# Optimization experiments

Hardware: AMD Instinct MI355X
Metric: run time of the kernel (lower is better)

Reference implementation:

```python
import jax, jax.numpy as jnp
import numpy as np
from jax import lax

N_TRACES = 128
TRACE_LEN = 32          # uniform trace length -> seq_len
INPUT_DIM = 64
HIDDEN_DIM = 128
BATCH = N_TRACES * TRACE_LEN  # 4096 events = batch_size


def setup_inputs() -> dict:
    key = jax.random.key(0)
    ks = jax.random.split(key, 12)
    s = 1.0 / np.sqrt(HIDDEN_DIM)
    u = lambda k, shape: jax.random.uniform(k, shape, jnp.float32, -s, s)
    return {
        "input": jax.random.normal(ks[0], (BATCH, INPUT_DIM), jnp.float32),
        # layer 0 LSTM params (gate order i,f,g,o as in torch)
        "W_ih0": u(ks[1], (4 * HIDDEN_DIM, INPUT_DIM)),
        "W_hh0": u(ks[2], (4 * HIDDEN_DIM, HIDDEN_DIM)),
        "b_ih0": u(ks[3], (4 * HIDDEN_DIM,)),
        "b_hh0": u(ks[4], (4 * HIDDEN_DIM,)),
        # layer 1 LSTM params
        "W_ih1": u(ks[5], (4 * HIDDEN_DIM, HIDDEN_DIM)),
        "W_hh1": u(ks[6], (4 * HIDDEN_DIM, HIDDEN_DIM)),
        "b_ih1": u(ks[7], (4 * HIDDEN_DIM,)),
        "b_hh1": u(ks[8], (4 * HIDDEN_DIM,)),
        # final linear: hidden -> 1
        "W_lin": u(ks[9], (1, HIDDEN_DIM)),
        "b_lin": u(ks[10], (1,)),
    }


def _lstm_layer(xs, W_ih, W_hh, b_ih, b_hh):
    # xs: [T, B, D_in] time-major. Returns hidden stream [T, B, H].
    H = W_hh.shape[1]
    B = xs.shape[1]
    # precompute input projection for all timesteps
    x_proj = jnp.einsum('tbd,gd->tbg', xs, W_ih) + b_ih + b_hh  # [T,B,4H]

    def step(carry, xp):
        h, c = carry
        gates = xp + h @ W_hh.T                # [B,4H]
        i, f, g, o = jnp.split(gates, 4, axis=-1)
        i = jax.nn.sigmoid(i)
        f = jax.nn.sigmoid(f)
        g = jnp.tanh(g)
        o = jax.nn.sigmoid(o)
        c = f * c + i * g
        h = o * jnp.tanh(c)
        return (h, c), h

    h0 = jnp.zeros((B, H), xs.dtype)
    _, hs = lax.scan(step, (h0, h0), x_proj)
    return hs


def _forward(input, W_ih0, W_hh0, b_ih0, b_hh0, W_ih1, W_hh1, b_ih1, b_hh1, W_lin, b_lin):
    L, D = TRACE_LEN, INPUT_DIM
    # Prefix scatter: event k of a trace gets the padded prefix events[0..k].
    x_tr = input.reshape(N_TRACES, L, D)                       # [Ntr, L, D]
    causal = (jnp.arange(L)[None, :] <= jnp.arange(L)[:, None])  # [k, j] mask j<=k
    padded = x_tr[:, None, :, :] * causal[None, :, :, None].astype(input.dtype)  # [Ntr,L(k),L(j),D]
    padded = padded.reshape(BATCH, L, D)                       # batch-first padded sequences

    xs = jnp.transpose(padded, (1, 0, 2))                      # [L, B, D] time-major
    h1 = _lstm_layer(xs, W_ih0, W_hh0, b_ih0, b_hh0)           # [L, B, H]
    h2 = _lstm_layer(h1, W_ih1, W_hh1, b_ih1, b_hh1)           # [L, B, H]

    out = jnp.einsum('tbh,oh->tbo', h2, W_lin) + b_lin         # [L, B, 1]
    # last valid timestep gather: lengths[i]-1 = (i mod L)
    lens_m1 = jnp.tile(jnp.arange(L), N_TRACES)                # [B]
    y_pred = out[lens_m1, jnp.arange(BATCH), 0]                # [B]
    return y_pred


def reference(input, W_ih0, W_hh0, b_ih0, b_hh0, W_ih1, W_hh1, b_ih1, b_hh1, W_lin, b_lin):
    return _forward(input, W_ih0, W_hh0, b_ih0, b_hh0, W_ih1, W_hh1, b_ih1, b_hh1, W_lin, b_lin)
```

## Files before the change

kernel.cpp:

```cpp
#include <hip/hip_runtime.h>

#define N_TRACES 128
#define TLEN 32
#define IN_DIM 64
#define HID 128
#define G4 (4 * HID)
#define BATCH (N_TRACES * TLEN)


__device__ __forceinline__ float fast_sigmoid(float x) {
    return 1.0f / (1.0f + __expf(-x));
}
__device__ __forceinline__ float fast_tanh(float x) {
    return 1.0f - 2.0f / (__expf(2.0f * x) + 1.0f);
}
__device__ __forceinline__ float quad_reduce(float x) {
    x += __int_as_float(__builtin_amdgcn_update_dpp(
        0, __float_as_int(x), 0xB1 , 0xF, 0xF, true));
    x += __int_as_float(__builtin_amdgcn_update_dpp(
        0, __float_as_int(x), 0x4E , 0xF, 0xF, true));
    return x;
}


template <int K>
__global__ __launch_bounds__(256) void gemm_bt(
    const float* __restrict__ A,
    const float* __restrict__ W,
    const float* __restrict__ b1,
    const float* __restrict__ b2,
    float* __restrict__ out,
    int Nld)
{
    constexpr int LD = 68;
    __shared__ float At[K][LD];
    __shared__ float Wt[K][LD];

    const int tid = threadIdx.x;
    const int m0 = blockIdx.x * 64;
    const int n0 = blockIdx.y * 64;

    #pragma unroll
    for (int j = 0; j < K / 16; ++j) {
        const int e = 4 * (tid + 256 * j);
        const int row = e / K;
        const int k = e % K;
        float4 va = *(const float4*)(A + (size_t)(m0 + row) * K + k);
        At[k + 0][row] = va.x; At[k + 1][row] = va.y;
        At[k + 2][row] = va.z; At[k + 3][row] = va.w;
        float4 vw = *(const float4*)(W + (size_t)(n0 + row) * K + k);
        Wt[k + 0][row] = vw.x; Wt[k + 1][row] = vw.y;
        Wt[k + 2][row] = vw.z; Wt[k + 3][row] = vw.w;
    }
    __syncthreads();

    const int tx = tid & 15;
    const int ty = tid >> 4;
    float acc[4][4] = {};

    #pragma unroll 4
    for (int k = 0; k < K; ++k) {
        float4 a = *(const float4*)&At[k][ty * 4];
        float4 w = *(const float4*)&Wt[k][tx * 4];
        acc[0][0] = fmaf(a.x, w.x, acc[0][0]); acc[0][1] = fmaf(a.x, w.y, acc[0][1]);
        acc[0][2] = fmaf(a.x, w.z, acc[0][2]); acc[0][3] = fmaf(a.x, w.w, acc[0][3]);
        acc[1][0] = fmaf(a.y, w.x, acc[1][0]); acc[1][1] = fmaf(a.y, w.y, acc[1][1]);
        acc[1][2] = fmaf(a.y, w.z, acc[1][2]); acc[1][3] = fmaf(a.y, w.w, acc[1][3]);
        acc[2][0] = fmaf(a.z, w.x, acc[2][0]); acc[2][1] = fmaf(a.z, w.y, acc[2][1]);
        acc[2][2] = fmaf(a.z, w.z, acc[2][2]); acc[2][3] = fmaf(a.z, w.w, acc[2][3]);
        acc[3][0] = fmaf(a.w, w.x, acc[3][0]); acc[3][1] = fmaf(a.w, w.y, acc[3][1]);
        acc[3][2] = fmaf(a.w, w.z, acc[3][2]); acc[3][3] = fmaf(a.w, w.w, acc[3][3]);
    }

    float bb[4];
    #pragma unroll
    for (int j = 0; j < 4; ++j) {
        const int n = n0 + tx * 4 + j;
        bb[j] = b1[n] + b2[n];
    }
    #pragma unroll
    for (int i = 0; i < 4; ++i) {
        const int m = m0 + ty * 4 + i;
        float4 v;
        v.x = acc[i][0] + bb[0]; v.y = acc[i][1] + bb[1];
        v.z = acc[i][2] + bb[2]; v.w = acc[i][3] + bb[3];
        *(float4*)(out + (size_t)m * Nld + n0 + tx * 4) = v;
    }
}


__global__ __launch_bounds__(512) void lstm_rec(
    const float* __restrict__ xproj,
    const float* __restrict__ Whh,
    float* __restrict__ hout)
{
    const int trace = blockIdx.x;
    const int tid = threadIdx.x;
    const int u = tid >> 2;
    const int s = tid & 3;

    float w[4][32];
    #pragma unroll
    for (int i = 0; i < 4; ++i) {
        const float* wr = Whh + (size_t)(u + 128 * i) * HID + 32 * s;
        #pragma unroll
        for (int j = 0; j < 8; ++j) {
            float4 v = *(const float4*)(wr + 4 * j);
            w[i][4 * j + 0] = v.x; w[i][4 * j + 1] = v.y;
            w[i][4 * j + 2] = v.z; w[i][4 * j + 3] = v.w;
        }
    }

    __shared__ float hbuf[2][144];
    if (tid < 144) { hbuf[0][tid] = 0.0f; hbuf[1][tid] = 0.0f; }

    const float* xpb = xproj + (size_t)trace * TLEN * G4;
    float* hob = hout + (size_t)trace * TLEN * HID;

    float xp[4] = {0.f, 0.f, 0.f, 0.f};
    if (s == 0) {
        #pragma unroll
        for (int i = 0; i < 4; ++i) xp[i] = xpb[u + 128 * i];
    }
    float c = 0.0f;
    __syncthreads();

    #pragma unroll 1
    for (int t = 0; t < TLEN; ++t) {
        const float* hb = &hbuf[t & 1][36 * s];
        float hv[32];
        #pragma unroll
        for (int j = 0; j < 8; ++j) {
            float4 v = *(const float4*)(hb + 4 * j);
            hv[4 * j + 0] = v.x; hv[4 * j + 1] = v.y;
            hv[4 * j + 2] = v.z; hv[4 * j + 3] = v.w;
        }

        float xn[4] = {0.f, 0.f, 0.f, 0.f};
        if (s == 0 && t + 1 < TLEN) {
            #pragma unroll
            for (int i = 0; i < 4; ++i) xn[i] = xpb[(t + 1) * G4 + u + 128 * i];
        }

        float acc0 = 0.f, acc1 = 0.f, acc2 = 0.f, acc3 = 0.f;
        #pragma unroll
        for (int j = 0; j < 32; ++j) {
            acc0 = fmaf(w[0][j], hv[j], acc0);
            acc1 = fmaf(w[1][j], hv[j], acc1);
            acc2 = fmaf(w[2][j], hv[j], acc2);
            acc3 = fmaf(w[3][j], hv[j], acc3);
        }
        acc0 = quad_reduce(acc0);
        acc1 = quad_reduce(acc1);
        acc2 = quad_reduce(acc2);
        acc3 = quad_reduce(acc3);

        if (s == 0) {
            const float iv = fast_sigmoid(acc0 + xp[0]);
            const float fv = fast_sigmoid(acc1 + xp[1]);
            const float gv = fast_tanh(acc2 + xp[2]);
            const float ov = fast_sigmoid(acc3 + xp[3]);
            c = fv * c + iv * gv;
            const float h = ov * fast_tanh(c);
            hbuf[(t + 1) & 1][u + 4 * (u >> 5)] = h;
            hob[t * HID + u] = h;
            xp[0] = xn[0]; xp[1] = xn[1]; xp[2] = xn[2]; xp[3] = xn[3];
        }
        __syncthreads();
    }
}


__global__ __launch_bounds__(256) void rowdot(
    const float* __restrict__ A,
    const float* __restrict__ wl,
    const float* __restrict__ bl,
    float* __restrict__ y)
{
    const int r = blockIdx.x * 256 + threadIdx.x;
    const float4* a4 = (const float4*)(A + (size_t)r * HID);
    const float4* w4 = (const float4*)wl;
    float sacc = 0.f;
    #pragma unroll
    for (int j = 0; j < HID / 4; ++j) {
        float4 a = a4[j], w = w4[j];
        sacc = fmaf(a.x, w.x, sacc);
        sacc = fmaf(a.y, w.y, sacc);
        sacc = fmaf(a.z, w.z, sacc);
        sacc = fmaf(a.w, w.w, sacc);
    }
    y[r] = sacc + bl[0];
}


extern "C" void kernel_launch(void* const* d_in, const int* in_sizes, int n_in,
                              void* d_out, int out_size, void* d_ws, size_t ws_size,
                              hipStream_t stream) {
    const float* input = (const float*)d_in[0];
    const float* W_ih0 = (const float*)d_in[1];
    const float* W_hh0 = (const float*)d_in[2];
    const float* b_ih0 = (const float*)d_in[3];
    const float* b_hh0 = (const float*)d_in[4];
    const float* W_ih1 = (const float*)d_in[5];
    const float* W_hh1 = (const float*)d_in[6];
    const float* b_ih1 = (const float*)d_in[7];
    const float* b_hh1 = (const float*)d_in[8];
    const float* W_lin = (const float*)d_in[9];
    const float* b_lin = (const float*)d_in[10];
    float* out = (float*)d_out;

    float* xproj = (float*)d_ws;
    float* h1 = xproj + (size_t)BATCH * G4;
    float* h2 = h1 + (size_t)BATCH * HID;

    dim3 ggrid(BATCH / 64, G4 / 64);

    gemm_bt<IN_DIM><<<ggrid, 256, 0, stream>>>(input, W_ih0, b_ih0, b_hh0, xproj, G4);
    lstm_rec<<<N_TRACES, 512, 0, stream>>>(xproj, W_hh0, h1);
    gemm_bt<HID><<<ggrid, 256, 0, stream>>>(h1, W_ih1, b_ih1, b_hh1, xproj, G4);
    lstm_rec<<<N_TRACES, 512, 0, stream>>>(xproj, W_hh1, h2);
    rowdot<<<BATCH / 256, 256, 0, stream>>>(h2, W_lin, b_lin, out);
}
```

Measured before the change: 180.2 us.

## Fuse both LSTM layers, layer-1 input projection and final linear into one per-trace kernel

Replaces the layer-0 recurrence, the layer-1 GEMM, the layer-1 recurrence and the rowdot with a single per-trace kernel. Hidden states and the layer-1 input projection stay in shared memory instead of going through global memory, and the separate launches go away. The GEMM's LDS transpose stores are also rotated per thread to reduce bank conflicts. The trade-off is that the layer-1 projection now runs as a matvec over only 128 blocks rather than a wide GEMM, and the kernel uses about 82KB of shared memory per block, which lowers occupancy.

Result: faster. 170.9 us (-5.1%).

```diff
diff --git a/kernel.cpp b/kernel.cpp
--- a/kernel.cpp
+++ b/kernel.cpp
@@ -20,6 +20,35 @@
     x += __int_as_float(__builtin_amdgcn_update_dpp(
         0, __float_as_int(x), 0x4E , 0xF, 0xF, true));
     return x;
+}
+
+__device__ __forceinline__ void load_w(const float* __restrict__ W, int u, int s,
+                                       float (&w)[4][32]) {
+    #pragma unroll
+    for (int i = 0; i < 4; ++i) {
+        const float* wr = W + (size_t)(u + 128 * i) * HID + 32 * s;
+        #pragma unroll
+        for (int j = 0; j < 8; ++j) {
+            float4 v = *(const float4*)(wr + 4 * j);
+            w[i][4 * j + 0] = v.x; w[i][4 * j + 1] = v.y;
+            w[i][4 * j + 2] = v.z; w[i][4 * j + 3] = v.w;
+        }
+    }
+}
+
+__device__ __forceinline__ void matvec_acc(const float (&w)[4][32],
+                                           const float* hb, float (&acc)[4]) {
+    #pragma unroll
+    for (int j = 0; j < 8; ++j) {
+        float4 v = *(const float4*)(hb + 4 * j);
+        float hx[4] = {v.x, v.y, v.z, v.w};
+        #pragma unroll
+        for (int e = 0; e < 4; ++e) {
+            #pragma unroll
+            for (int i = 0; i < 4; ++i)
+                acc[i] = fmaf(w[i][4 * j + e], hx[e], acc[i]);
+        }
+    }
 }
 
 
@@ -40,17 +69,22 @@
     const int m0 = blockIdx.x * 64;
     const int n0 = blockIdx.y * 64;
 
+    const int rot = tid & 3;
     #pragma unroll
     for (int j = 0; j < K / 16; ++j) {
         const int e = 4 * (tid + 256 * j);
         const int row = e / K;
         const int k = e % K;
         float4 va = *(const float4*)(A + (size_t)(m0 + row) * K + k);
-        At[k + 0][row] = va.x; At[k + 1][row] = va.y;
-        At[k + 2][row] = va.z; At[k + 3][row] = va.w;
         float4 vw = *(const float4*)(W + (size_t)(n0 + row) * K + k);
-        Wt[k + 0][row] = vw.x; Wt[k + 1][row] = vw.y;
-        Wt[k + 2][row] = vw.z; Wt[k + 3][row] = vw.w;
+        float fa[4] = {va.x, va.y, va.z, va.w};
+        float fw[4] = {vw.x, vw.y, vw.z, vw.w};
+        #pragma unroll
+        for (int ii = 0; ii < 4; ++ii) {
+            const int i = (ii + rot) & 3;
+            At[k + i][row] = fa[i];
+            Wt[k + i][row] = fw[i];
+        }
     }
     __syncthreads();
 
@@ -89,107 +123,123 @@
 }
 
 
-__global__ __launch_bounds__(512) void lstm_rec(
-    const float* __restrict__ xproj,
-    const float* __restrict__ Whh,
-    float* __restrict__ hout)
+__global__ __launch_bounds__(512, 2) void fused_trace(
+    const float* __restrict__ xproj0,
+    const float* __restrict__ Whh0,
+    const float* __restrict__ Wih1,
+    const float* __restrict__ bih1,
+    const float* __restrict__ bhh1,
+    const float* __restrict__ Whh1,
+    const float* __restrict__ Wlin,
+    const float* __restrict__ blin,
+    float* __restrict__ y)
 {
     const int trace = blockIdx.x;
     const int tid = threadIdx.x;
     const int u = tid >> 2;
     const int s = tid & 3;
+    const int pu = u + 4 * (u >> 5);
+
+    __shared__ float hs[TLEN][140];
+    __shared__ float xp1[TLEN][G4];
 
     float w[4][32];
-    #pragma unroll
-    for (int i = 0; i < 4; ++i) {
-        const float* wr = Whh + (size_t)(u + 128 * i) * HID + 32 * s;
-        #pragma unroll
-        for (int j = 0; j < 8; ++j) {
-            float4 v = *(const float4*)(wr + 4 * j);
-            w[i][4 * j + 0] = v.x; w[i][4 * j + 1] = v.y;
-            w[i][4 * j + 2] = v.z; w[i][4 * j + 3] = v.w;
-        }
-    }
-
-    __shared__ float hbuf[2][144];
-    if (tid < 144) { hbuf[0][tid] = 0.0f; hbuf[1][tid] = 0.0f; }
-
-    const float* xpb = xproj + (size_t)trace * TLEN * G4;
-    float* hob = hout + (size_t)trace * TLEN * HID;
-
+
+    load_w(Whh0, u, s, w);
+    const float* xpb = xproj0 + (size_t)trace * TLEN * G4;
     float xp[4] = {0.f, 0.f, 0.f, 0.f};
     if (s == 0) {
         #pragma unroll
         for (int i = 0; i < 4; ++i) xp[i] = xpb[u + 128 * i];
     }
     float c = 0.0f;
-    __syncthreads();
-
     #pragma unroll 1
     for (int t = 0; t < TLEN; ++t) {
-        const float* hb = &hbuf[t & 1][36 * s];
-        float hv[32];
-        #pragma unroll
-        for (int j = 0; j < 8; ++j) {
-            float4 v = *(const float4*)(hb + 4 * j);
-            hv[4 * j + 0] = v.x; hv[4 * j + 1] = v.y;
-            hv[4 * j + 2] = v.z; hv[4 * j + 3] = v.w;
-        }
+        float acc[4] = {0.f, 0.f, 0.f, 0.f};
+        if (t > 0) matvec_acc(w, &hs[t - 1][36 * s], acc);
 
         float xn[4] = {0.f, 0.f, 0.f, 0.f};
         if (s == 0 && t + 1 < TLEN) {
             #pragma unroll
             for (int i = 0; i < 4; ++i) xn[i] = xpb[(t + 1) * G4 + u + 128 * i];
         }
-
-        float acc0 = 0.f, acc1 = 0.f, acc2 = 0.f, acc3 = 0.f;
-        #pragma unroll
-        for (int j = 0; j < 32; ++j) {
-            acc0 = fmaf(w[0][j], hv[j], acc0);
-            acc1 = fmaf(w[1][j], hv[j], acc1);
-            acc2 = fmaf(w[2][j], hv[j], acc2);
-            acc3 = fmaf(w[3][j], hv[j], acc3);
-        }
-        acc0 = quad_reduce(acc0);
-        acc1 = quad_reduce(acc1);
-        acc2 = quad_reduce(acc2);
-        acc3 = quad_reduce(acc3);
+        #pragma unroll
+        for (int i = 0; i < 4; ++i) acc[i] = quad_reduce(acc[i]);
 
         if (s == 0) {
-            const float iv = fast_sigmoid(acc0 + xp[0]);
-            const float fv = fast_sigmoid(acc1 + xp[1]);
-            const float gv = fast_tanh(acc2 + xp[2]);
-            const float ov = fast_sigmoid(acc3 + xp[3]);
+            const float iv = fast_sigmoid(acc[0] + xp[0]);
+            const float fv = fast_sigmoid(acc[1] + xp[1]);
+            const float gv = fast_tanh(acc[2] + xp[2]);
+            const float ov = fast_sigmoid(acc[3] + xp[3]);
             c = fv * c + iv * gv;
-            const float h = ov * fast_tanh(c);
-            hbuf[(t + 1) & 1][u + 4 * (u >> 5)] = h;
-            hob[t * HID + u] = h;
+            hs[t][pu] = ov * fast_tanh(c);
             xp[0] = xn[0]; xp[1] = xn[1]; xp[2] = xn[2]; xp[3] = xn[3];
         }
         __syncthreads();
     }
-}
-
-
-__global__ __launch_bounds__(256) void rowdot(
-    const float* __restrict__ A,
-    const float* __restrict__ wl,
-    const float* __restrict__ bl,
-    float* __restrict__ y)
-{
-    const int r = blockIdx.x * 256 + threadIdx.x;
-    const float4* a4 = (const float4*)(A + (size_t)r * HID);
-    const float4* w4 = (const float4*)wl;
-    float sacc = 0.f;
-    #pragma unroll
-    for (int j = 0; j < HID / 4; ++j) {
-        float4 a = a4[j], w = w4[j];
-        sacc = fmaf(a.x, w.x, sacc);
-        sacc = fmaf(a.y, w.y, sacc);
-        sacc = fmaf(a.z, w.z, sacc);
-        sacc = fmaf(a.w, w.w, sacc);
-    }
-    y[r] = sacc + bl[0];
+
+    load_w(Wih1, u, s, w);
+    float bi[4] = {0.f, 0.f, 0.f, 0.f};
+    if (s == 0) {
+        #pragma unroll
+        for (int i = 0; i < 4; ++i) bi[i] = bih1[u + 128 * i] + bhh1[u + 128 * i];
+    }
+    #pragma unroll 1
+    for (int t = 0; t < TLEN; ++t) {
+        float acc[4] = {0.f, 0.f, 0.f, 0.f};
+        matvec_acc(w, &hs[t][36 * s], acc);
+        #pragma unroll
+        for (int i = 0; i < 4; ++i) acc[i] = quad_reduce(acc[i]);
+        if (s == 0) {
+            #pragma unroll
+            for (int i = 0; i < 4; ++i) xp1[t][u + 128 * i] = acc[i] + bi[i];
+        }
+    }
+    __syncthreads();
+
+    load_w(Whh1, u, s, w);
+    c = 0.0f;
+    #pragma unroll 1
+    for (int t = 0; t < TLEN; ++t) {
+        float acc[4] = {0.f, 0.f, 0.f, 0.f};
+        if (t > 0) matvec_acc(w, &hs[t - 1][36 * s], acc);
+        #pragma unroll
+        for (int i = 0; i < 4; ++i) acc[i] = quad_reduce(acc[i]);
+
+        if (s == 0) {
+            const float iv = fast_sigmoid(acc[0] + xp1[t][u]);
+            const float fv = fast_sigmoid(acc[1] + xp1[t][u + 128]);
+            const float gv = fast_tanh(acc[2] + xp1[t][u + 256]);
+            const float ov = fast_sigmoid(acc[3] + xp1[t][u + 384]);
+            c = fv * c + iv * gv;
+            hs[t][pu] = ov * fast_tanh(c);
+        }
+        __syncthreads();
+    }
+
+    if (tid < 128) {
+        const int tq = tid >> 2;
+        const int sq = tid & 3;
+        float wl[32];
+        #pragma unroll
+        for (int j = 0; j < 8; ++j) {
+            float4 v = *(const float4*)(Wlin + 32 * sq + 4 * j);
+            wl[4 * j + 0] = v.x; wl[4 * j + 1] = v.y;
+            wl[4 * j + 2] = v.z; wl[4 * j + 3] = v.w;
+        }
+        const float* hb = &hs[tq][36 * sq];
+        float a = 0.f;
+        #pragma unroll
+        for (int j = 0; j < 8; ++j) {
+            float4 v = *(const float4*)(hb + 4 * j);
+            a = fmaf(v.x, wl[4 * j + 0], a);
+            a = fmaf(v.y, wl[4 * j + 1], a);
+            a = fmaf(v.z, wl[4 * j + 2], a);
+            a = fmaf(v.w, wl[4 * j + 3], a);
+        }
+        a = quad_reduce(a);
+        if (sq == 0) y[trace * TLEN + tq] = a + blin[0];
+    }
 }
 
 
@@ -209,15 +259,11 @@
     const float* b_lin = (const float*)d_in[10];
     float* out = (float*)d_out;
 
-    float* xproj = (float*)d_ws;
-    float* h1 = xproj + (size_t)BATCH * G4;
-    float* h2 = h1 + (size_t)BATCH * HID;
+    float* xproj0 = (float*)d_ws;
 
     dim3 ggrid(BATCH / 64, G4 / 64);
 
-    gemm_bt<IN_DIM><<<ggrid, 256, 0, stream>>>(input, W_ih0, b_ih0, b_hh0, xproj, G4);
-    lstm_rec<<<N_TRACES, 512, 0, stream>>>(xproj, W_hh0, h1);
-    gemm_bt<HID><<<ggrid, 256, 0, stream>>>(h1, W_ih1, b_ih1, b_hh1, xproj, G4);
-    lstm_rec<<<N_TRACES, 512, 0, stream>>>(xproj, W_hh1, h2);
-    rowdot<<<BATCH / 256, 256, 0, stream>>>(h2, W_lin, b_lin, out);
-}
+    gemm_bt<IN_DIM><<<ggrid, 256, 0, stream>>>(input, W_ih0, b_ih0, b_hh0, xproj0, G4);
+    fused_trace<<<N_TRACES, 512, 0, stream>>>(xproj0, W_hh0, W_ih1, b_ih1, b_hh1,
+                                              W_hh1, W_lin, b_lin, out);
+}
```
